# Optimization experiments

Hardware: AMD Instinct MI355X
Metric: run time of the kernel (lower is better)

The kernel has to match this reference:

```python
import jax, jax.numpy as jnp
import numpy as np
import functools, math

HEADS = 16


def _query_chunk_attention(query, key, value, precision, key_chunk_size=4096):
    # query: (q_chunk, bh, d); key/value: (kv, bh, d)
    num_kv, num_heads, k_features = key.shape[-3:]
    v_features = value.shape[-1]
    key_chunk_size = min(key_chunk_size, num_kv)
    query = query / jnp.sqrt(k_features)

    @functools.partial(jax.checkpoint, prevent_cse=False)
    def summarize_chunk(query, key, value):
        attn_weights = jnp.einsum("...qhd,...khd->...qhk", query, key, precision=precision)
        max_score = jnp.max(attn_weights, axis=-1, keepdims=True)
        max_score = jax.lax.stop_gradient(max_score)
        exp_weights = jnp.exp(attn_weights - max_score)
        exp_values = jnp.einsum("...vhf,...qhv->...qhf", value, exp_weights, precision=precision)
        max_score = jnp.einsum("...qhk->...qh", max_score)
        return exp_values, exp_weights.sum(axis=-1), max_score

    def chunk_scanner(chunk_idx):
        key_chunk = jax.lax.dynamic_slice(
            key, [chunk_idx, 0, 0], [key_chunk_size, num_heads, k_features])
        value_chunk = jax.lax.dynamic_slice(
            value, [chunk_idx, 0, 0], [key_chunk_size, num_heads, v_features])
        return summarize_chunk(query, key_chunk, value_chunk)

    chunk_values, chunk_weights, chunk_max = jax.lax.map(
        chunk_scanner, xs=jnp.arange(0, num_kv, key_chunk_size))
    # online softmax rescaling across kv chunks
    global_max = jnp.max(chunk_max, axis=0, keepdims=True)
    max_diffs = jnp.exp(chunk_max - global_max)
    chunk_values = chunk_values * jnp.expand_dims(max_diffs, axis=-1)
    chunk_weights = chunk_weights * max_diffs
    all_values = chunk_values.sum(axis=0)
    all_weights = jnp.expand_dims(chunk_weights, -1).sum(axis=0)
    return all_values / all_weights


def jax_memory_efficient_attention(query, key, value,
                                   precision=jax.lax.Precision.HIGHEST,
                                   query_chunk_size=1024, key_chunk_size=4096):
    # query: (q_len, bh, d)
    num_q, num_heads, q_features = query.shape[-3:]

    def chunk_scanner(chunk_idx, _):
        query_chunk = jax.lax.dynamic_slice(
            query, [chunk_idx, 0, 0],
            [min(query_chunk_size, num_q), num_heads, q_features])
        return (chunk_idx + query_chunk_size,
                _query_chunk_attention(query_chunk, key, value, precision, key_chunk_size))

    _, res = jax.lax.scan(chunk_scanner, 0, xs=None,
                          length=math.ceil(num_q / query_chunk_size))
    return jnp.concatenate(res, axis=-3)


def _reshape_heads_to_batch_dim(tensor, heads):
    b, s, d = tensor.shape
    t = tensor.reshape(b, s, heads, d // heads).transpose(0, 2, 1, 3)
    return t.reshape(b * heads, s, d // heads)


def _attention_fwd(query, key, value):
    heads = HEADS
    q = _reshape_heads_to_batch_dim(query, heads).transpose(1, 0, 2)  # (s, b*h, dh)
    k = _reshape_heads_to_batch_dim(key, heads).transpose(1, 0, 2)
    v = _reshape_heads_to_batch_dim(value, heads).transpose(1, 0, 2)
    flatten_latent_dim = q.shape[-3]
    if flatten_latent_dim % 64 == 0:
        query_chunk_size = flatten_latent_dim // 64
    elif flatten_latent_dim % 16 == 0:
        query_chunk_size = flatten_latent_dim // 16
    elif flatten_latent_dim % 4 == 0:
        query_chunk_size = flatten_latent_dim // 4
    else:
        query_chunk_size = flatten_latent_dim
    out = jax_memory_efficient_attention(q, k, v,
                                         query_chunk_size=query_chunk_size,
                                         key_chunk_size=4096 * 4)
    return out.transpose(1, 0, 2)  # (b*h, s, dh)


def setup_inputs() -> dict:
    key = jax.random.key(0)
    k1, k2, k3 = jax.random.split(key, 3)
    B, S, D = 2, 4096, 1024
    return {
        "query": jax.random.normal(k1, (B, S, D), dtype=jnp.float32),
        "key": jax.random.normal(k2, (B, S, D), dtype=jnp.float32),
        "value": jax.random.normal(k3, (B, S, D), dtype=jnp.float32),
    }


def reference(query, key, value):
    return _attention_fwd(query, key, value)
```

## Files before the change

kernel.cpp:

```cpp
#include <hip/hip_runtime.h>
#include <math.h>

#define SEQ    4096
#define DH     64
#define DMODEL 1024
#define NBH    32
#define NT64   64
#define LOG2E  1.44269504088896340736f

typedef __attribute__((ext_vector_type(8)))  short short8;
typedef __attribute__((ext_vector_type(4)))  float f32x4;
typedef __attribute__((ext_vector_type(16))) float f32x16;
typedef __attribute__((ext_vector_type(2)))  unsigned uint2v;

#define WS_KV_BYTES   33554432ull
#define WS_NEED_SPLIT 68157440ull

__device__ __forceinline__ unsigned short f2bf(float f) {
  union { float f; unsigned u; } x; x.f = f;
  unsigned r = x.u + 0x7FFFu + ((x.u >> 16) & 1u);
  return (unsigned short)(r >> 16);
}
__device__ __forceinline__ float bf2f(unsigned short u) {
  union { unsigned u; float f; } x; x.u = ((unsigned)u) << 16;
  return x.f;
}
__device__ __forceinline__ unsigned cvtpk_bf16(float lo, float hi) {
  unsigned r;
  asm("v_cvt_pk_bf16_f32 %0, %1, %2" : "=v"(r) : "v"(lo), "v"(hi));
  return r;
}

__global__ __launch_bounds__(256)
void prep(const float* __restrict__ Kp, const float* __restrict__ Vp,
          unsigned short* __restrict__ ws) {
  __shared__ unsigned short Kt[128 * DH];
  __shared__ unsigned short Vt[128 * DH];
  const int blk = blockIdx.x;
  const int bh = blk >> 5, t128 = blk & 31;
  const int b = bh >> 4, h = bh & 15;
  const size_t gbase = (size_t)b * SEQ * DMODEL + (size_t)h * DH +
                       (size_t)t128 * 128 * DMODEL;
  const float* Kb = Kp + gbase;
  const float* Vb = Vp + gbase;
  unsigned short* wt = ws + (size_t)bh * NT64 * 8192 + (size_t)(2 * t128) * 8192;
  const int tid = threadIdx.x;

#pragma unroll
  for (int c = 0; c < 8; ++c) {
    const int idx = c * 256 + tid;
    const int row = idx >> 4, dc = idx & 15;
    f32x4 kf = *(const f32x4*)(Kb + (size_t)row * DMODEL + dc * 4);
    f32x4 vf = *(const f32x4*)(Vb + (size_t)row * DMODEL + dc * 4);
    uint2v ku, vu;
    ku[0] = (unsigned)f2bf(kf[0]) | ((unsigned)f2bf(kf[1]) << 16);
    ku[1] = (unsigned)f2bf(kf[2]) | ((unsigned)f2bf(kf[3]) << 16);
    vu[0] = (unsigned)f2bf(vf[0]) | ((unsigned)f2bf(vf[1]) << 16);
    vu[1] = (unsigned)f2bf(vf[2]) | ((unsigned)f2bf(vf[3]) << 16);
    *(uint2v*)&Kt[row * 64 + dc * 4] = ku;
    *(uint2v*)&Vt[row * 64 + dc * 4] = vu;
  }
  __syncthreads();

#pragma unroll
  for (int c = 0; c < 4; ++c) {
    const int idx = c * 256 + tid;
    const int l31 = idx & 31, hi = (idx >> 5) & 1, d4 = (idx >> 6) & 3, kb = idx >> 8;
    const int tau = kb >> 1, kb2 = kb & 1;
    short8 v = *(const short8*)&Kt[(kb * 32 + l31) * 64 + d4 * 16 + hi * 8];
    *(short8*)&wt[tau * 8192 + (((kb2 * 4 + d4) * 2 + hi) * 32 + l31) * 8] = v;
  }
#pragma unroll
  for (int c = 0; c < 4; ++c) {
    const int idx = c * 256 + tid;
    const int l31 = idx & 31, dt = (idx >> 5) & 1, hi = (idx >> 6) & 1, k16 = idx >> 7;
    const int tau = k16 >> 2, k162 = k16 & 3;
    const int d = dt * 32 + l31, kb0 = k16 * 16 + hi * 8;
    short8 v;
#pragma unroll
    for (int j = 0; j < 8; ++j) v[j] = (short)Vt[(kb0 + j) * 64 + d];
    *(short8*)&wt[tau * 8192 + 4096 + (((k162 * 2 + hi) * 64) + dt * 32 + l31) * 8] = v;
  }
}

__device__ __forceinline__ f32x16 qk_block(const char* Lk, int kbpar, int laneK,
                                           const short8* qb, const f32x16& ZERO) {
  short8 ka0 = *(const short8*)(Lk + kbpar * 4096 + 0 * 1024 + laneK);
  short8 ka1 = *(const short8*)(Lk + kbpar * 4096 + 1 * 1024 + laneK);
  short8 ka2 = *(const short8*)(Lk + kbpar * 4096 + 2 * 1024 + laneK);
  short8 ka3 = *(const short8*)(Lk + kbpar * 4096 + 3 * 1024 + laneK);
  f32x16 z;
  z = __builtin_amdgcn_mfma_f32_32x32x16_bf16(ka0, qb[0], ZERO, 0, 0, 0);
  z = __builtin_amdgcn_mfma_f32_32x32x16_bf16(ka1, qb[1], z, 0, 0, 0);
  z = __builtin_amdgcn_mfma_f32_32x32x16_bf16(ka2, qb[2], z, 0, 0, 0);
  z = __builtin_amdgcn_mfma_f32_32x32x16_bf16(ka3, qb[3], z, 0, 0, 0);
  return z;
}

__device__ __forceinline__ void proc_block(f32x16& z, const char* Lv, int k16base,
                                           int laneV, f32x16& accL, f32x16& accH,
                                           float& lsum) {
#pragma unroll
  for (int r = 0; r < 16; ++r) z[r] = __builtin_amdgcn_exp2f(z[r]);
  {
    float s0 = (z[0] + z[1]) + (z[2] + z[3]);
    float s1 = (z[4] + z[5]) + (z[6] + z[7]);
    float s2 = (z[8] + z[9]) + (z[10] + z[11]);
    float s3 = (z[12] + z[13]) + (z[14] + z[15]);
    lsum += (s0 + s1) + (s2 + s3);
  }
#pragma unroll
  for (int s = 0; s < 2; ++s) {
    const int R = 8 * s;
    unsigned a0 = cvtpk_bf16(z[R + 0], z[R + 1]);
    unsigned c0 = cvtpk_bf16(z[R + 4], z[R + 5]);
    unsigned a1 = cvtpk_bf16(z[R + 2], z[R + 3]);
    unsigned c1 = cvtpk_bf16(z[R + 6], z[R + 7]);
    asm("v_permlane32_swap_b32 %0, %1" : "+v"(a0), "+v"(c0));
    asm("v_permlane32_swap_b32 %0, %1" : "+v"(a1), "+v"(c1));
    union { unsigned u[4]; short8 s8; } pw;
    pw.u[0] = a0; pw.u[1] = a1; pw.u[2] = c0; pw.u[3] = c1;
    const int k16 = k16base + s;
    short8 vb0 = *(const short8*)(Lv + k16 * 2048 + laneV);
    short8 vb1 = *(const short8*)(Lv + k16 * 2048 + 512 + laneV);
    accL = __builtin_amdgcn_mfma_f32_32x32x16_bf16(pw.s8, vb0, accL, 0, 0, 0);
    accH = __builtin_amdgcn_mfma_f32_32x32x16_bf16(pw.s8, vb1, accH, 0, 0, 0);
  }
}

template <bool SPLIT>
__global__ __launch_bounds__(256, 4)
void fattn(const float* __restrict__ Qp,
           const unsigned short* __restrict__ ws,
           float* __restrict__ Op) {
  __shared__ __align__(16) char lds[2][16384];

  const int tid  = threadIdx.x;
  const int lane = tid & 63;
  const int w    = tid >> 6;
  const int hi   = lane >> 5;
  const int l31  = lane & 31;

  int bh, qc, sh, rid;
  if (SPLIT) {
    const int id = blockIdx.x;
    rid = (id & 7) * 256 + (id >> 3);
    bh = rid >> 6; qc = (rid >> 1) & 31; sh = rid & 1;
  } else {
    const int id = blockIdx.x;
    rid = (id & 7) * 128 + (id >> 3);
    bh = rid >> 5; qc = rid & 31; sh = 0;
  }
  const int NTloc = SPLIT ? 32 : 64;
  const int t0    = sh * 32;
  const int q0    = qc * 128 + w * 32;

  const int b = bh >> 4, h = bh & 15;
  const float* Qb = Qp + (size_t)b * SEQ * DMODEL + (size_t)h * DH;
  const char* wsb = (const char*)(ws + (size_t)bh * NT64 * 8192);

  short8 qb[4];
  {
    const float* qr = Qb + (size_t)(q0 + l31) * DMODEL;
    const float sc = 0.125f * LOG2E;
#pragma unroll
    for (int d4 = 0; d4 < 4; ++d4) {
      const float* p = qr + d4 * 16 + hi * 8;
      f32x4 f0 = *(const f32x4*)p;
      f32x4 f1 = *(const f32x4*)(p + 4);
      short8 v;
#pragma unroll
      for (int i = 0; i < 4; ++i) {
        v[i]     = (short)f2bf(f0[i] * sc);
        v[i + 4] = (short)f2bf(f1[i] * sc);
      }
      qb[d4] = v;
    }
  }

  f32x16 ZERO;
#pragma unroll
  for (int r = 0; r < 16; ++r) ZERO[r] = 0.f;
  f32x16 accL = ZERO, accH = ZERO;
  float lsum = 0.f;

  const int laneK = hi * 512 + l31 * 16;
  const int laneV = hi * 1024 + l31 * 16;

#define STAGE(buf_, tau_)                                                     \
  {                                                                           \
    const char* src_ = wsb + (size_t)(tau_) * 16384;                          \
    char* dst_ = &lds[buf_][0];                                               \
    _Pragma("unroll")                                                         \
    for (int c_ = 0; c_ < 4; ++c_) {                                          \
      __builtin_amdgcn_global_load_lds(                                       \
          (const __attribute__((address_space(1))) void*)(src_ + c_ * 4096 +  \
                                                          tid * 16),          \
          (__attribute__((address_space(3))) void*)(dst_ + c_ * 4096 +        \
                                                    tid * 16),                \
          16, 0, 0);                                                          \
    }                                                                         \
  }

  STAGE(0, t0);
  __syncthreads();

  f32x16 zE, zO;
  for (int t = 0; t < NTloc; ++t) {
    const int cur = t & 1;
    const char* Lk  = &lds[cur][0];
    const char* Lv  = &lds[cur][8192];
    const char* LvO = &lds[cur ^ 1][8192];

    zE = qk_block(Lk, 0, laneK, qb, ZERO);
    if (t > 0)
      proc_block(zO, LvO, 2, laneV, accL, accH, lsum);
    __syncthreads();
    if (t + 1 < NTloc) STAGE(cur ^ 1, t0 + t + 1);
    zO = qk_block(Lk, 1, laneK, qb, ZERO);
    proc_block(zE, Lv, 0, laneV, accL, accH, lsum);
    __syncthreads();
  }
  proc_block(zO, &lds[(NTloc - 1) & 1][8192], 2, laneV, accL, accH, lsum);

  if (SPLIT) {
    unsigned short* part =
        (unsigned short*)((char*)const_cast<unsigned short*>(ws) + WS_KV_BYTES) +
        (size_t)rid * 8192;
    float* lout = (float*)((char*)const_cast<unsigned short*>(ws) +
                           2 * WS_KV_BYTES) + (size_t)rid * 128;
    const float lt = lsum + __shfl_xor(lsum, 32, 64);
    if (hi == 0) lout[w * 32 + l31] = lt;
#pragma unroll
    for (int r = 0; r < 16; ++r) {
      const int qrow = (r & 3) + 8 * (r >> 2) + 4 * hi;
      part[(w * 32 + qrow) * 64 + l31]      = f2bf(accL[r]);
      part[(w * 32 + qrow) * 64 + 32 + l31] = f2bf(accH[r]);
    }
  } else {
    const float lt  = lsum + __shfl_xor(lsum, 32, 64);
    const float inv = 1.0f / lt;
#pragma unroll
    for (int r = 0; r < 16; ++r) {
      const int qrow = (r & 3) + 8 * (r >> 2) + 4 * hi;
      const float iv = __shfl(inv, qrow + (lane & 32), 64);
      const size_t row = (size_t)bh * SEQ + q0 + qrow;
      Op[row * DH + l31]      = accL[r] * iv;
      Op[row * DH + 32 + l31] = accH[r] * iv;
    }
  }
#undef STAGE
}

__global__ __launch_bounds__(256)
void combine(const unsigned short* __restrict__ ws, float* __restrict__ Op) {
  const unsigned short* part = (const unsigned short*)((const char*)ws + WS_KV_BYTES);
  const float* lsum = (const float*)((const char*)ws + 2 * WS_KV_BYTES);
  const int gid = blockIdx.x * 256 + threadIdx.x;
  const int bqc = gid >> 10;
  const int rem = gid & 1023;
  const int q = rem >> 3, dc = rem & 7;
  const int pid0 = bqc * 2, pid1 = pid0 + 1;
  short8 A0 = *(const short8*)&part[(size_t)pid0 * 8192 + q * 64 + dc * 8];
  short8 A1 = *(const short8*)&part[(size_t)pid1 * 8192 + q * 64 + dc * 8];
  const float l = lsum[pid0 * 128 + q] + lsum[pid1 * 128 + q];
  const float inv = 1.0f / l;
  const int bh = bqc >> 5, qc = bqc & 31;
  float* o = Op + ((size_t)bh * SEQ + qc * 128 + q) * DH + dc * 8;
  f32x4 o0, o1;
#pragma unroll
  for (int j = 0; j < 4; ++j) {
    o0[j] = (bf2f((unsigned short)A0[j]) + bf2f((unsigned short)A1[j])) * inv;
    o1[j] = (bf2f((unsigned short)A0[j + 4]) + bf2f((unsigned short)A1[j + 4])) * inv;
  }
  *(f32x4*)o = o0;
  *(f32x4*)(o + 4) = o1;
}

extern "C" void kernel_launch(void* const* d_in, const int* in_sizes, int n_in,
                              void* d_out, int out_size, void* d_ws, size_t ws_size,
                              hipStream_t stream) {
  const float* Q = (const float*)d_in[0];
  const float* K = (const float*)d_in[1];
  const float* V = (const float*)d_in[2];
  float* O = (float*)d_out;
  unsigned short* ws = (unsigned short*)d_ws;

  prep<<<dim3(NBH * 32), dim3(256), 0, stream>>>(K, V, ws);
  if (ws_size >= WS_NEED_SPLIT) {
    fattn<true><<<dim3(2048), dim3(256), 0, stream>>>(Q, ws, O);
    combine<<<dim3(4096), dim3(256), 0, stream>>>(ws, O);
  } else {
    fattn<false><<<dim3(1024), dim3(256), 0, stream>>>(Q, ws, O);
  }
}
```

Measured before the change: 168.3 us.

## Drop KV split and combine pass; triple-buffer LDS with single barrier per tile

Removes the two-way KV split path and its bf16 partial/combine kernel, so each block processes all 64 KV tiles and normalizes directly. LDS goes from double to triple buffering, with explicit vmcnt waits and one barrier per iteration instead of two, and prefetch runs two tiles ahead. QK and PV are now computed sequentially per half-tile instead of interleaved across halves. Fewer blocks (1024 vs 2048) and lower occupancy (3 vs 4 blocks per CU) risk reduced parallelism on the CUs.

```diff
diff --git a/kernel.cpp b/kernel.cpp
--- a/kernel.cpp
+++ b/kernel.cpp
@@ -13,17 +13,10 @@
 typedef __attribute__((ext_vector_type(16))) float f32x16;
 typedef __attribute__((ext_vector_type(2)))  unsigned uint2v;
 
-#define WS_KV_BYTES   33554432ull
-#define WS_NEED_SPLIT 68157440ull
-
 __device__ __forceinline__ unsigned short f2bf(float f) {
   union { float f; unsigned u; } x; x.f = f;
   unsigned r = x.u + 0x7FFFu + ((x.u >> 16) & 1u);
   return (unsigned short)(r >> 16);
-}
-__device__ __forceinline__ float bf2f(unsigned short u) {
-  union { unsigned u; float f; } x; x.u = ((unsigned)u) << 16;
-  return x.f;
 }
 __device__ __forceinline__ unsigned cvtpk_bf16(float lo, float hi) {
   unsigned r;
@@ -128,12 +121,11 @@
   }
 }
 
-template <bool SPLIT>
-__global__ __launch_bounds__(256, 4)
+__global__ __launch_bounds__(256, 3)
 void fattn(const float* __restrict__ Qp,
            const unsigned short* __restrict__ ws,
            float* __restrict__ Op) {
-  __shared__ __align__(16) char lds[2][16384];
+  __shared__ __align__(16) char lds[3 * 16384];
 
   const int tid  = threadIdx.x;
   const int lane = tid & 63;
@@ -141,19 +133,11 @@
   const int hi   = lane >> 5;
   const int l31  = lane & 31;
 
-  int bh, qc, sh, rid;
-  if (SPLIT) {
-    const int id = blockIdx.x;
-    rid = (id & 7) * 256 + (id >> 3);
-    bh = rid >> 6; qc = (rid >> 1) & 31; sh = rid & 1;
-  } else {
-    const int id = blockIdx.x;
-    rid = (id & 7) * 128 + (id >> 3);
-    bh = rid >> 5; qc = rid & 31; sh = 0;
-  }
-  const int NTloc = SPLIT ? 32 : 64;
-  const int t0    = sh * 32;
-  const int q0    = qc * 128 + w * 32;
+  const int id  = blockIdx.x;
+  const int rid = (id & 7) * 128 + (id >> 3);
+  const int bh  = rid >> 5;
+  const int qc  = rid & 31;
+  const int q0  = qc * 128 + w * 32;
 
   const int b = bh >> 4, h = bh & 15;
   const float* Qb = Qp + (size_t)b * SEQ * DMODEL + (size_t)h * DH;
@@ -187,10 +171,10 @@
   const int laneK = hi * 512 + l31 * 16;
   const int laneV = hi * 1024 + l31 * 16;
 
-#define STAGE(buf_, tau_)                                                     \
+#define STAGE(dsto_, tau_)                                                    \
   {                                                                           \
     const char* src_ = wsb + (size_t)(tau_) * 16384;                          \
-    char* dst_ = &lds[buf_][0];                                               \
+    char* dst_ = &lds[dsto_];                                                 \
     _Pragma("unroll")                                                         \
     for (int c_ = 0; c_ < 4; ++c_) {                                          \
       __builtin_amdgcn_global_load_lds(                                       \
@@ -202,79 +186,44 @@
     }                                                                         \
   }
 
-  STAGE(0, t0);
-  __syncthreads();
-
-  f32x16 zE, zO;
-  for (int t = 0; t < NTloc; ++t) {
-    const int cur = t & 1;
-    const char* Lk  = &lds[cur][0];
-    const char* Lv  = &lds[cur][8192];
-    const char* LvO = &lds[cur ^ 1][8192];
-
-    zE = qk_block(Lk, 0, laneK, qb, ZERO);
-    if (t > 0)
-      proc_block(zO, LvO, 2, laneV, accL, accH, lsum);
-    __syncthreads();
-    if (t + 1 < NTloc) STAGE(cur ^ 1, t0 + t + 1);
-    zO = qk_block(Lk, 1, laneK, qb, ZERO);
-    proc_block(zE, Lv, 0, laneV, accL, accH, lsum);
-    __syncthreads();
-  }
-  proc_block(zO, &lds[(NTloc - 1) & 1][8192], 2, laneV, accL, accH, lsum);
-
-  if (SPLIT) {
-    unsigned short* part =
-        (unsigned short*)((char*)const_cast<unsigned short*>(ws) + WS_KV_BYTES) +
-        (size_t)rid * 8192;
-    float* lout = (float*)((char*)const_cast<unsigned short*>(ws) +
-                           2 * WS_KV_BYTES) + (size_t)rid * 128;
-    const float lt = lsum + __shfl_xor(lsum, 32, 64);
-    if (hi == 0) lout[w * 32 + l31] = lt;
-#pragma unroll
-    for (int r = 0; r < 16; ++r) {
-      const int qrow = (r & 3) + 8 * (r >> 2) + 4 * hi;
-      part[(w * 32 + qrow) * 64 + l31]      = f2bf(accL[r]);
-      part[(w * 32 + qrow) * 64 + 32 + l31] = f2bf(accH[r]);
+  int oA = 0, oB = 16384, oC = 32768;
+  STAGE(oA, 0);
+  STAGE(oB, 1);
+
+  for (int t = 0; t < NT64; ++t) {
+    if (t < NT64 - 1) {
+      asm volatile("s_waitcnt vmcnt(4)" ::: "memory");
+    } else {
+      asm volatile("s_waitcnt vmcnt(0)" ::: "memory");
     }
-  } else {
-    const float lt  = lsum + __shfl_xor(lsum, 32, 64);
-    const float inv = 1.0f / lt;
-#pragma unroll
-    for (int r = 0; r < 16; ++r) {
-      const int qrow = (r & 3) + 8 * (r >> 2) + 4 * hi;
-      const float iv = __shfl(inv, qrow + (lane & 32), 64);
-      const size_t row = (size_t)bh * SEQ + q0 + qrow;
-      Op[row * DH + l31]      = accL[r] * iv;
-      Op[row * DH + 32 + l31] = accH[r] * iv;
+    __builtin_amdgcn_sched_barrier(0);
+    __builtin_amdgcn_s_barrier();
+    __builtin_amdgcn_sched_barrier(0);
+
+    if (t + 2 < NT64) STAGE(oC, t + 2);
+
+    const char* Lk = &lds[oA];
+    const char* Lv = &lds[oA + 8192];
+#pragma unroll
+    for (int kb = 0; kb < 2; ++kb) {
+      f32x16 z = qk_block(Lk, kb, laneK, qb, ZERO);
+      proc_block(z, Lv, kb * 2, laneV, accL, accH, lsum);
     }
+
+    const int tmp = oA; oA = oB; oB = oC; oC = tmp;
+  }
+
+  const float lt  = lsum + __shfl_xor(lsum, 32, 64);
+  const float inv = 1.0f / lt;
+#pragma unroll
+  for (int r = 0; r < 16; ++r) {
+    const int qrow = (r & 3) + 8 * (r >> 2) + 4 * hi;
+    const float iv = __shfl(inv, qrow + (lane & 32), 64);
+    const size_t row = (size_t)bh * SEQ + q0 + qrow;
+    Op[row * DH + l31]      = accL[r] * iv;
+    Op[row * DH + 32 + l31] = accH[r] * iv;
   }
 #undef STAGE
-}
-
-__global__ __launch_bounds__(256)
-void combine(const unsigned short* __restrict__ ws, float* __restrict__ Op) {
-  const unsigned short* part = (const unsigned short*)((const char*)ws + WS_KV_BYTES);
-  const float* lsum = (const float*)((const char*)ws + 2 * WS_KV_BYTES);
-  const int gid = blockIdx.x * 256 + threadIdx.x;
-  const int bqc = gid >> 10;
-  const int rem = gid & 1023;
-  const int q = rem >> 3, dc = rem & 7;
-  const int pid0 = bqc * 2, pid1 = pid0 + 1;
-  short8 A0 = *(const short8*)&part[(size_t)pid0 * 8192 + q * 64 + dc * 8];
-  short8 A1 = *(const short8*)&part[(size_t)pid1 * 8192 + q * 64 + dc * 8];
-  const float l = lsum[pid0 * 128 + q] + lsum[pid1 * 128 + q];
-  const float inv = 1.0f / l;
-  const int bh = bqc >> 5, qc = bqc & 31;
-  float* o = Op + ((size_t)bh * SEQ + qc * 128 + q) * DH + dc * 8;
-  f32x4 o0, o1;
-#pragma unroll
-  for (int j = 0; j < 4; ++j) {
-    o0[j] = (bf2f((unsigned short)A0[j]) + bf2f((unsigned short)A1[j])) * inv;
-    o1[j] = (bf2f((unsigned short)A0[j + 4]) + bf2f((unsigned short)A1[j + 4])) * inv;
-  }
-  *(f32x4*)o = o0;
-  *(f32x4*)(o + 4) = o1;
 }
 
 extern "C" void kernel_launch(void* const* d_in, const int* in_sizes, int n_in,
@@ -287,10 +236,5 @@
   unsigned short* ws = (unsigned short*)d_ws;
 
   prep<<<dim3(NBH * 32), dim3(256), 0, stream>>>(K, V, ws);
-  if (ws_size >= WS_NEED_SPLIT) {
-    fattn<true><<<dim3(2048), dim3(256), 0, stream>>>(Q, ws, O);
-    combine<<<dim3(4096), dim3(256), 0, stream>>>(ws, O);
-  } else {
-    fattn<false><<<dim3(1024), dim3(256), 0, stream>>>(Q, ws, O);
-  }
-}
+  fattn<<<dim3(1024), dim3(256), 0, stream>>>(Q, ws, O);
+}
```

Measured after the change: 159.5 us. 5.2% less time.
